# Optimization experiments

Measured on AMD Instinct MI355X. Metric: run time of the kernel, lower is better.

The kernel has to match this reference:

```python
import math
import jax, jax.numpy as jnp
import numpy as np

B, T, D, K = 8, 2048, 1024, 4096  # batch, seq, d_model, num_audio_tokens


def _positional_encoding(seq_len, d_model):
    position = jnp.arange(seq_len, dtype=jnp.float32)[:, None]
    div_term = jnp.exp(jnp.arange(0, d_model, 2, dtype=jnp.float32) * (-math.log(10000.0) / d_model))
    pe = jnp.zeros((seq_len, d_model), dtype=jnp.float32)
    pe = pe.at[:, 0::2].set(jnp.sin(position * div_term))
    pe = pe.at[:, 1::2].set(jnp.cos(position * div_term))
    return pe


def setup_inputs() -> dict:
    key = jax.random.key(0)
    k1, k2, k3 = jax.random.split(key, 3)
    x = jax.random.normal(k1, (B, T, D), dtype=jnp.float32)
    # codebook: nn.initializers.normal() default stddev = 0.01
    codebook = jax.random.normal(k2, (K, D), dtype=jnp.float32) * 0.01
    # nn.Embed table for quantized tokens
    embed_table = jax.random.normal(k3, (K, D), dtype=jnp.float32) * 0.02
    return {"x": x, "codebook": codebook, "embed_table": embed_table}


def reference(x, codebook, embed_table):
    # VQ branch: argmin over L2 distance to codebook.
    x2 = jnp.sum(x * x, axis=-1, keepdims=True)          # [B,T,1]
    c2 = jnp.sum(codebook * codebook, axis=-1)           # [K]
    xc = jnp.einsum('btd,kd->btk', x, codebook)          # [B,T,K]
    d2 = x2 - 2.0 * xc + c2                              # [B,T,K]
    indices = jnp.argmin(d2, axis=-1)                    # [B,T]
    q = embed_table[indices]                             # [B,T,D] gather
    pe = _positional_encoding(T, D)                      # [T,D]
    return q + pe[None, :, :]
```

## Files before the change

### kernel.cpp

```cpp
#include <hip/hip_runtime.h>
#include <hip/hip_bf16.h>
#include <cstddef>

#define BB 8
#define TT 2048
#define DD 1024
#define KK 4096
#define MM (BB * TT)

#define WMARG 1.0e-6
#define EPROBE 2.0e-6
#define NFIN 4

#define LEX_LT(v,i,w,j) ((v) < (w) || ((v) == (w) && (i) < (j)))

typedef unsigned long long u64;
typedef __attribute__((ext_vector_type(8))) short short8;
typedef __attribute__((ext_vector_type(8))) unsigned short ushort8v;
typedef __attribute__((ext_vector_type(4))) float f32x4;

#define AS1 __attribute__((address_space(1)))
#define AS3 __attribute__((address_space(3)))

__device__ __forceinline__ u64 u64min(u64 a, u64 b) { return a < b ? a : b; }
__device__ __forceinline__ u64 u64max(u64 a, u64 b) { return a > b ? a : b; }

__device__ __forceinline__ unsigned short f2bu(float f) {
    __hip_bfloat16 h = __float2bfloat16(f);
    union { __hip_bfloat16 b; unsigned short u; } cv; cv.b = h; return cv.u;
}
__device__ __forceinline__ unsigned fmono(float f) {
    unsigned b = __float_as_uint(f);
    return (b & 0x80000000u) ? ~b : (b | 0x80000000u);
}

__device__ __forceinline__ float4 pe_add(float4 ev, int m, int c4) {
    const float tf  = (float)(m % TT);
    const float NEG = -9.210340371976184f / 1024.0f;
    int d = c4 * 4;
    float f0 = expf((float)d * NEG);
    float f2 = expf((float)(d + 2) * NEG);
    float a0 = tf * f0, a2 = tf * f2;
    float4 r;
    r.x = ev.x + sinf(a0);
    r.y = ev.y + cosf(a0);
    r.z = ev.z + sinf(a2);
    r.w = ev.w + cosf(a2);
    return r;
}

__global__ __launch_bounds__(256)
void prep_kernel(const float* __restrict__ xsrc, unsigned short* __restrict__ xdh,
                 float* __restrict__ xss,
                 const float* __restrict__ csrc, unsigned short* __restrict__ cdh,
                 float* __restrict__ css) {
    const int lane = threadIdx.x & 63;
    const int wave = (blockIdx.x * 256 + threadIdx.x) >> 6;
    int row  = wave * 8 + (lane >> 3);
    const int blk  = lane & 7;

    const float* a;
    unsigned short* hp;
    float* sumsq;
    if (row < MM) {
        a = xsrc + (size_t)row * DD + blk * 128;
        hp = xdh + (size_t)row * DD + blk * 128;
        sumsq = xss + row;
    } else {
        int r2 = row - MM;
        a = csrc + (size_t)r2 * DD + blk * 128;
        hp = cdh + (size_t)r2 * DD + blk * 128;
        sumsq = css + r2;
    }

    float r[8];
    #pragma unroll
    for (int g = 0; g < 16; ++g) {
        float4 v0 = *(const float4*)(a + g * 8);
        float4 v1 = *(const float4*)(a + g * 8 + 4);
        float e[8] = {v0.x, v0.y, v0.z, v0.w, v1.x, v1.y, v1.z, v1.w};
        ushort8v hv;
        #pragma unroll
        for (int j = 0; j < 8; ++j) {
            hv[j] = f2bu(e[j]);
            float sq = __fmul_rn(e[j], e[j]);
            r[j] = (g == 0) ? sq : __fadd_rn(r[j], sq);
        }
        *(ushort8v*)(hp + g * 8) = hv;
    }
    float b = __fadd_rn(__fadd_rn(__fadd_rn(r[0], r[1]), __fadd_rn(r[2], r[3])),
                        __fadd_rn(__fadd_rn(r[4], r[5]), __fadd_rn(r[6], r[7])));
    float t = __fadd_rn(b, __shfl_xor(b, 1, 64));
    float u = __fadd_rn(t, __shfl_xor(t, 2, 64));
    float s = __fadd_rn(u, __shfl_xor(u, 4, 64));
    if (blk == 0) *sumsq = s;
}

__global__ __launch_bounds__(512)
void vq_gemm_kernel(const unsigned short* __restrict__ xh,
                    const unsigned short* __restrict__ cbh,
                    const float* __restrict__ c2,
                    u64* __restrict__ cand2) {
    __shared__ char smem[49152];
    unsigned short (*Ah)[64] = (unsigned short(*)[64])(smem);
    unsigned short (*Bh)[64] = (unsigned short(*)[64])(smem + 32768);

    const int t    = threadIdx.x;
    const int lane = t & 63;
    const int w    = t >> 6;
    const int wr   = w >> 1;
    const int wc   = w & 1;
    const int m0   = blockIdx.x * 256;
    const int n0   = blockIdx.y * 128;

    const int l8  = lane >> 3;
    const int lsw = (lane & 7) ^ l8;
    const char* gA = (const char*)xh  + (size_t)(m0 + w * 32 + l8) * (DD * 2) + (size_t)lsw * 16;
    const char* gB = (const char*)cbh + (size_t)(n0 + w * 16 + l8) * (DD * 2) + (size_t)lsw * 16;

    f32x4 acc[4][4];
    #pragma unroll
    for (int i = 0; i < 4; ++i)
        #pragma unroll
        for (int j = 0; j < 4; ++j) acc[i][j] = (f32x4)0.f;

    for (int kt = 0; kt < 16; ++kt) {
        const size_t kOffB = (size_t)kt * 128;

        __syncthreads();
        #pragma unroll
        for (int i = 0; i < 4; ++i) {
            __builtin_amdgcn_global_load_lds(
                (const AS1 void*)(gA + (size_t)(i * 8) * (DD * 2) + kOffB),
                (AS3 void*)((char*)&Ah[w * 32 + i * 8][0]), 16, 0, 0);
        }
        #pragma unroll
        for (int i = 0; i < 2; ++i) {
            __builtin_amdgcn_global_load_lds(
                (const AS1 void*)(gB + (size_t)(i * 8) * (DD * 2) + kOffB),
                (AS3 void*)((char*)&Bh[w * 16 + i * 8][0]), 16, 0, 0);
        }
        __syncthreads();

        #pragma unroll
        for (int kf = 0; kf < 2; ++kf) {
            const int bidx = kf * 4 + (lane >> 4);
            const int swz  = (bidx ^ (lane & 7)) * 8;
            short8 ah[4];
            #pragma unroll
            for (int mf = 0; mf < 4; ++mf)
                ah[mf] = *(const short8*)&Ah[wr * 64 + mf * 16 + (lane & 15)][swz];
            #pragma unroll
            for (int nf = 0; nf < 4; ++nf) {
                short8 bh = *(const short8*)&Bh[wc * 64 + nf * 16 + (lane & 15)][swz];
                #pragma unroll
                for (int mf = 0; mf < 4; ++mf)
                    acc[mf][nf] = __builtin_amdgcn_mfma_f32_16x16x32_bf16(ah[mf], bh, acc[mf][nf], 0, 0, 0);
            }
        }
    }

    float (*sc)[16][68] = (float(*)[16][68])(smem);

    #pragma unroll
    for (int mf = 0; mf < 4; ++mf) {
        __syncthreads();
        #pragma unroll
        for (int nf = 0; nf < 4; ++nf)
            #pragma unroll
            for (int j = 0; j < 4; ++j)
                sc[w][(lane >> 4) * 4 + j][nf * 16 + (lane & 15)] = acc[mf][nf][j];
        __syncthreads();

        const int lr  = t >> 3;
        const int seg = t & 7;
        const int wrr = lr >> 4;
        const int r16 = lr & 15;
        const int wv  = wrr * 2 + (seg >> 2);
        const int cb0 = (seg & 3) * 16;
        const int kb  = n0 + seg * 16;
        u64 k0 = ~0ULL, k1 = ~0ULL;
        #pragma unroll
        for (int i = 0; i < 16; ++i) {
            float s = c2[kb + i] - 2.0f * sc[wv][r16][cb0 + i];
            u64 key = (((u64)fmono(s)) << 32) | (unsigned)(kb + i);
            if (key < k1) {
                if (key < k0) { k1 = k0; k0 = key; }
                else          { k1 = key; }
            }
        }
        #pragma unroll
        for (int off = 1; off < 8; off <<= 1) {
            u64 b0 = __shfl_xor(k0, off, 64);
            u64 b1 = __shfl_xor(k1, off, 64);
            u64 n0k = u64min(k0, b0);
            u64 n1k = u64min(u64max(k0, b0), u64min(k1, b1));
            k0 = n0k; k1 = n1k;
        }
        if (seg == 0) {
            int m = m0 + wrr * 64 + mf * 16 + r16;
            cand2[(size_t)(blockIdx.y * 2 + 0) * MM + m] = k0;
            cand2[(size_t)(blockIdx.y * 2 + 1) * MM + m] = k1;
        }
    }
}

__device__ __forceinline__ float ulpf(float v) {
    unsigned u = __float_as_uint(v) & 0x7f800000u;
    return __uint_as_float(u) * 1.1920928955078125e-7f;
}
__device__ __forceinline__ float chain_qv(float x2v, float xc, float c2k) {
    return __fadd_rn(__fsub_rn(x2v, __fmul_rn(2.0f, xc)), c2k);
}

__global__ __launch_bounds__(256)
void vq_select_out_kernel(const u64* __restrict__ cand2,
                          const float* __restrict__ x, const float* __restrict__ cb,
                          const float* __restrict__ x2, const float* __restrict__ c2,
                          const float* __restrict__ embed, float* __restrict__ out,
                          int* __restrict__ sel_idx, int* __restrict__ alt_idx,
                          u64* __restrict__ best) {
    const int m   = blockIdx.x;
    const int tid = threadIdx.x;
    __shared__ float sx[DD];
    __shared__ int   gk[NFIN];
    __shared__ float gq[NFIN], galt[NFIN], gmarg[NFIN];
    __shared__ int   gi[NFIN];
    __shared__ int   schosen;

    ((float4*)sx)[tid] = ((const float4*)(x + (size_t)m * DD))[tid];

    if (tid < 64) {
        u64 a = cand2[(size_t)tid * MM + m];
        #pragma unroll
        for (int s = 0; s < NFIN; ++s) {
            u64 mn = a;
            #pragma unroll
            for (int off = 32; off > 0; off >>= 1) {
                u64 o = __shfl_xor(mn, off, 64);
                mn = (o < mn) ? o : mn;
            }
            if (tid == 0) gk[s] = (int)(mn & 0xffffffffu);
            if (a == mn) a = ~0ULL;
        }
    }
    __syncthreads();

    const int c   = tid >> 6;
    const int sub = tid & 63;
    const int k   = gk[c];
    const float* __restrict__ crow = cb + (size_t)k * DD;
    double dbl = 0.0;
    #pragma unroll
    for (int j = 0; j < DD / 64; ++j) {
        int i = sub + j * 64;
        dbl = fma((double)sx[i], (double)crow[i], dbl);
    }
    #pragma unroll
    for (int off = 32; off > 0; off >>= 1) dbl += __shfl_xor(dbl, off, 64);

    if (sub == 0) {
        const float x2m = x2[m], c2k = c2[k];
        const float xc  = (float)dbl;
        double v_sub = (double)x2m - 2.0 * (double)xc;
        float  s     = (float)v_sub;
        double v_add = (double)s + (double)c2k;
        float  qv    = (float)v_add;
        double d_sub = 0.5 * (double)ulpf(s)  - fabs(v_sub - (double)s);
        double d_add = 0.5 * (double)ulpf(qv) - fabs(v_add - (double)qv);
        double marg  = fmin(d_sub, d_add) * 0.5;

        float qm = chain_qv(x2m, (float)(dbl - EPROBE), c2k);
        float qp = chain_qv(x2m, (float)(dbl + EPROBE), c2k);
        float qa = qv;
        if (qm != qv) qa = qm;
        else if (qp != qv) qa = qp;

        gq[c] = qv; gi[c] = k; galt[c] = qa;
        gmarg[c] = (marg < WMARG && qa != qv) ? (float)marg : 1e30f;
    }
    __syncthreads();

    if (tid == 0) {
        float bv = gq[0]; int bi = gi[0];
        for (int t = 1; t < NFIN; ++t)
            if (LEX_LT(gq[t], gi[t], bv, bi)) { bv = gq[t]; bi = gi[t]; }

        float bestm = 1e30f; int altwin = bi;
        for (int t = 0; t < NFIN; ++t) {
            if (gmarg[t] >= 1e29f) continue;
            float wv = (0 == t) ? galt[0] : gq[0]; int wi = gi[0];
            for (int s2 = 1; s2 < NFIN; ++s2) {
                float v = (s2 == t) ? galt[s2] : gq[s2];
                if (LEX_LT(v, gi[s2], wv, wi)) { wv = v; wi = gi[s2]; }
            }
            if (wi != bi && gmarg[t] < bestm) { bestm = gmarg[t]; altwin = wi; }
        }
        sel_idx[m] = bi;
        alt_idx[m] = altwin;
        schosen = bi;
        if (altwin != bi) {
            u64 key = ((u64)__float_as_uint(bestm) << 32) | (unsigned)m;
            atomicMin(best, key);
        }
    }
    __syncthreads();

    const int idx = schosen;
    float4 ev = ((const float4*)(embed + (size_t)idx * DD))[tid];
    ((float4*)(out + (size_t)m * DD))[tid] = pe_add(ev, m, tid);
}

__global__ __launch_bounds__(256)
void vq_fixup_kernel(const int* __restrict__ sel_idx, const int* __restrict__ alt_idx,
                     const u64* __restrict__ best,
                     const float* __restrict__ embed, float* __restrict__ out) {
    u64 key = *best;
    if (key == ~0ULL) return;
    const int m   = (int)(key & 0xffffffffu);
    const int idx = alt_idx[m];
    if (idx == sel_idx[m]) return;
    const int tid = threadIdx.x;
    float4 ev = ((const float4*)(embed + (size_t)idx * DD))[tid];
    ((float4*)(out + (size_t)m * DD))[tid] = pe_add(ev, m, tid);
}

extern "C" void kernel_launch(void* const* d_in, const int* in_sizes, int n_in,
                              void* d_out, int out_size, void* d_ws, size_t ws_size,
                              hipStream_t stream) {
    const float* x     = (const float*)d_in[0];
    const float* cb    = (const float*)d_in[1];
    const float* embed = (const float*)d_in[2];
    float* out = (float*)d_out;

    char* wp = (char*)d_ws;
    u64* best            = (u64*)wp;                       wp += 16;
    u64* cand2           = (u64*)wp;                       wp += (size_t)64 * MM * 8;
    unsigned short* cbh  = (unsigned short*)wp;            wp += (size_t)KK * DD * 2;
    unsigned short* xh   = (unsigned short*)wp;            wp += (size_t)MM * DD * 2;
    float* c2            = (float*)wp;                     wp += (size_t)KK * 4;
    float* x2            = (float*)wp;                     wp += (size_t)MM * 4;
    int*   sel_idx       = (int*)wp;                       wp += (size_t)MM * 4;
    int*   alt_idx       = (int*)wp;

    hipMemsetAsync(best, 0xFF, 8, stream);

    prep_kernel<<<(MM + KK) / 32, 256, 0, stream>>>(x, xh, x2, cb, cbh, c2);

    dim3 grid(MM / 256, KK / 128);
    vq_gemm_kernel<<<grid, 512, 0, stream>>>(xh, cbh, c2, cand2);

    vq_select_out_kernel<<<MM, 256, 0, stream>>>(cand2, x, cb, x2, c2,
                                                 embed, out, sel_idx, alt_idx, best);

    vq_fixup_kernel<<<1, 256, 0, stream>>>(sel_idx, alt_idx, best, embed, out);
}
```

Baseline: 280.3 us.

## Double-buffer GEMM LDS tiles with halved K-step and raised compute priority

Restructures the bf16 MFMA distance GEMM main loop into a double-buffered pipeline. Each step now loads the next 32-wide K slice into the alternate LDS buffer while MFMAs run on the current one, with a new swizzle for the 64-byte rows. Wave priority is raised around the compute section. This removes one barrier per iteration and overlaps global-to-LDS loads with compute, but doubles the number of loop iterations and makes each step smaller.

Result: slower. 303.8 us (+8.4%).

```diff
diff --git a/kernel.cpp b/kernel.cpp
--- a/kernel.cpp
+++ b/kernel.cpp
@@ -102,8 +102,6 @@
                     const float* __restrict__ c2,
                     u64* __restrict__ cand2) {
     __shared__ char smem[49152];
-    unsigned short (*Ah)[64] = (unsigned short(*)[64])(smem);
-    unsigned short (*Bh)[64] = (unsigned short(*)[64])(smem + 32768);
 
     const int t    = threadIdx.x;
     const int lane = t & 63;
@@ -113,10 +111,10 @@
     const int m0   = blockIdx.x * 256;
     const int n0   = blockIdx.y * 128;
 
-    const int l8  = lane >> 3;
-    const int lsw = (lane & 7) ^ l8;
-    const char* gA = (const char*)xh  + (size_t)(m0 + w * 32 + l8) * (DD * 2) + (size_t)lsw * 16;
-    const char* gB = (const char*)cbh + (size_t)(n0 + w * 16 + l8) * (DD * 2) + (size_t)lsw * 16;
+    const int l4  = lane >> 2;
+    const int lsw = (lane & 3) ^ (l4 & 3);
+    const char* gA = (const char*)xh  + (size_t)(m0 + w * 32 + l4) * (DD * 2) + (size_t)lsw * 16;
+    const char* gB = (const char*)cbh + (size_t)(n0 + w * 16 + l4) * (DD * 2) + (size_t)lsw * 16;
 
     f32x4 acc[4][4];
     #pragma unroll
@@ -124,40 +122,48 @@
         #pragma unroll
         for (int j = 0; j < 4; ++j) acc[i][j] = (f32x4)0.f;
 
-    for (int kt = 0; kt < 16; ++kt) {
-        const size_t kOffB = (size_t)kt * 128;
-
-        __syncthreads();
-        #pragma unroll
-        for (int i = 0; i < 4; ++i) {
-            __builtin_amdgcn_global_load_lds(
-                (const AS1 void*)(gA + (size_t)(i * 8) * (DD * 2) + kOffB),
-                (AS3 void*)((char*)&Ah[w * 32 + i * 8][0]), 16, 0, 0);
-        }
+    auto STAGE = [&](int buf, int kt) {
+        char* bufA = smem + buf * 24576;
+        char* bufB = bufA + 16384;
+        const size_t kOffB = (size_t)kt * 64;
         #pragma unroll
         for (int i = 0; i < 2; ++i) {
             __builtin_amdgcn_global_load_lds(
-                (const AS1 void*)(gB + (size_t)(i * 8) * (DD * 2) + kOffB),
-                (AS3 void*)((char*)&Bh[w * 16 + i * 8][0]), 16, 0, 0);
-        }
-        __syncthreads();
-
-        #pragma unroll
-        for (int kf = 0; kf < 2; ++kf) {
-            const int bidx = kf * 4 + (lane >> 4);
-            const int swz  = (bidx ^ (lane & 7)) * 8;
-            short8 ah[4];
+                (const AS1 void*)(gA + (size_t)(i * 16) * (DD * 2) + kOffB),
+                (AS3 void*)(bufA + (size_t)(w * 32 + i * 16) * 64), 16, 0, 0);
+        }
+        __builtin_amdgcn_global_load_lds(
+            (const AS1 void*)(gB + kOffB),
+            (AS3 void*)(bufB + (size_t)(w * 16) * 64), 16, 0, 0);
+    };
+
+    auto COMPUTE = [&](int buf) {
+        unsigned short (*Ah)[32] = (unsigned short(*)[32])(smem + buf * 24576);
+        unsigned short (*Bh)[32] = (unsigned short(*)[32])(smem + buf * 24576 + 16384);
+        const int swz = ((lane >> 4) ^ (lane & 3)) * 8;
+        short8 ah[4];
+        #pragma unroll
+        for (int mf = 0; mf < 4; ++mf)
+            ah[mf] = *(const short8*)&Ah[wr * 64 + mf * 16 + (lane & 15)][swz];
+        #pragma unroll
+        for (int nf = 0; nf < 4; ++nf) {
+            short8 bh = *(const short8*)&Bh[wc * 64 + nf * 16 + (lane & 15)][swz];
             #pragma unroll
             for (int mf = 0; mf < 4; ++mf)
-                ah[mf] = *(const short8*)&Ah[wr * 64 + mf * 16 + (lane & 15)][swz];
-            #pragma unroll
-            for (int nf = 0; nf < 4; ++nf) {
-                short8 bh = *(const short8*)&Bh[wc * 64 + nf * 16 + (lane & 15)][swz];
-                #pragma unroll
-                for (int mf = 0; mf < 4; ++mf)
-                    acc[mf][nf] = __builtin_amdgcn_mfma_f32_16x16x32_bf16(ah[mf], bh, acc[mf][nf], 0, 0, 0);
-            }
-        }
+                acc[mf][nf] = __builtin_amdgcn_mfma_f32_16x16x32_bf16(ah[mf], bh, acc[mf][nf], 0, 0, 0);
+        }
+    };
+
+    STAGE(0, 0);
+    __syncthreads();
+
+    for (int kt = 0; kt < 32; ++kt) {
+        const int cur = kt & 1;
+        if (kt < 31) STAGE(cur ^ 1, kt + 1);
+        __builtin_amdgcn_s_setprio(1);
+        COMPUTE(cur);
+        __builtin_amdgcn_s_setprio(0);
+        __syncthreads();
     }
 
     float (*sc)[16][68] = (float(*)[16][68])(smem);
@@ -283,18 +289,18 @@
 
     if (tid == 0) {
         float bv = gq[0]; int bi = gi[0];
-        for (int t = 1; t < NFIN; ++t)
-            if (LEX_LT(gq[t], gi[t], bv, bi)) { bv = gq[t]; bi = gi[t]; }
+        for (int t2 = 1; t2 < NFIN; ++t2)
+            if (LEX_LT(gq[t2], gi[t2], bv, bi)) { bv = gq[t2]; bi = gi[t2]; }
 
         float bestm = 1e30f; int altwin = bi;
-        for (int t = 0; t < NFIN; ++t) {
-            if (gmarg[t] >= 1e29f) continue;
-            float wv = (0 == t) ? galt[0] : gq[0]; int wi = gi[0];
+        for (int t2 = 0; t2 < NFIN; ++t2) {
+            if (gmarg[t2] >= 1e29f) continue;
+            float wv = (0 == t2) ? galt[0] : gq[0]; int wi = gi[0];
             for (int s2 = 1; s2 < NFIN; ++s2) {
-                float v = (s2 == t) ? galt[s2] : gq[s2];
+                float v = (s2 == t2) ? galt[s2] : gq[s2];
                 if (LEX_LT(v, gi[s2], wv, wi)) { wv = v; wi = gi[s2]; }
             }
-            if (wi != bi && gmarg[t] < bestm) { bestm = gmarg[t]; altwin = wi; }
+            if (wi != bi && gmarg[t2] < bestm) { bestm = gmarg[t2]; altwin = wi; }
         }
         sel_idx[m] = bi;
         alt_idx[m] = altwin;
```
